# Kernel optimization log

Hardware: AMD Instinct MI355X
Metric: run time of the kernel (lower is better)

The kernel has to match this reference:

```python
import jax, jax.numpy as jnp
from jax import lax
import numpy as np

B, T, NCLS, D = 64, 2048, 20, 2048
LCS_LEN, FSD_LEN = 64, 32
LAMB1, LAMB2, LAMB3 = 1.0, 5e-5, 8e-5
LAMB_LCS, LAMB_FSD = 0.01, 0.01
FEAT_MARGIN = 50.0
THRES = 0.5
GAMMA = 0.1


def cos_sim(a, b):
    a = a / jnp.linalg.norm(a, axis=1, keepdims=True)
    b = b / jnp.linalg.norm(b, axis=1, keepdims=True)
    return a @ b.T


def dp_fsd(c0, c1):
    # soft-LCS/DTW-style recurrence with maxGamma (soft max) over 3 neighbors
    h = c0.shape[-1] // 2
    m = cos_sim(c0[:, :h], c1[:, :h])  # [L, L]
    g = cos_sim(c0[:, h:], c1[:, h:])  # [L, L]
    L = m.shape[0]

    def row_step(prev_row, mg):
        m_row, g_row = mg
        diag = prev_row[:-1]  # C[i-1, j-1]
        up = prev_row[1:]     # C[i-1, j]

        def col_step(left, xs):  # left = C[i, j-1]
            d, u, mij, gij = xs
            neigh = jnp.stack([d, gij + u, gij + left])
            val = mij + GAMMA * jax.nn.logsumexp(neigh / GAMMA)
            return val, val

        _, row_vals = lax.scan(col_step, jnp.zeros((), m.dtype), (diag, up, m_row, g_row))
        new_row = jnp.concatenate([jnp.zeros((1,), m.dtype), row_vals])
        return new_row, None

    final_row, _ = lax.scan(row_step, jnp.zeros(L + 1, m.dtype), (m, g))
    return final_row[-1]


def dp_lcs(c0, c1):
    s = cos_sim(c0, c1)  # [L, L]
    L = s.shape[0]

    def row_step(prev_row, s_row):
        diag = prev_row[:-1]
        up = prev_row[1:]

        def col_step(left, xs):
            d, u, sij = xs
            val = jnp.where(sij > THRES, d + sij, jnp.maximum(u, left))
            return val, val

        _, row_vals = lax.scan(col_step, jnp.zeros((), s.dtype), (diag, up, s_row))
        return jnp.concatenate([jnp.zeros((1,), s.dtype), row_vals]), None

    final_row, _ = lax.scan(row_step, jnp.zeros(L + 1, s.dtype), s)
    return final_row[-1]


def cls_criterion(p, lab):
    return -jnp.mean(jnp.sum(jnp.log(p + 1e-10) * lab, axis=1))


def forward_once(ai_cls, ac_cls, ab_cls, vlab, att, ai_feat, ac_feat, ab_feat, ai_cas):
    bs = ai_cls.shape[0]
    ones = jnp.ones((bs, 1), ai_cls.dtype)
    zeros = jnp.zeros((bs, 1), ai_cls.dtype)
    inst_lab = jnp.concatenate([vlab, zeros], axis=1)
    cont_lab = jnp.concatenate([vlab, ones], axis=1)
    back_lab = jnp.concatenate([jnp.zeros_like(vlab), ones], axis=1)
    inst_lab = inst_lab / jnp.sum(inst_lab, axis=1, keepdims=True)
    cont_lab = cont_lab / jnp.sum(cont_lab, axis=1, keepdims=True)
    back_lab = back_lab / jnp.sum(back_lab, axis=1, keepdims=True)

    inst_loss = cls_criterion(ai_cls, inst_lab)
    cont_loss = cls_criterion(ac_cls, cont_lab)
    back_loss = cls_criterion(ab_cls, back_lab)

    guide_loss = jnp.mean(jnp.sum(jnp.abs(1.0 - ai_cas[:, :, -1] - lax.stop_gradient(att[:, :, 0])), axis=1))

    n_inst = jnp.linalg.norm(ai_feat, axis=1)
    n_cont = jnp.linalg.norm(ac_feat, axis=1)
    n_back = jnp.linalg.norm(ab_feat, axis=1)
    f1 = jnp.maximum(FEAT_MARGIN - n_inst + n_cont, 0.0)
    f2 = jnp.maximum(FEAT_MARGIN - n_cont + n_back, 0.0)
    f3 = n_back
    feat_loss = jnp.mean((f1 + f2 + f3) ** 2)

    sparse_loss = jnp.mean(jnp.sum(att[:, :, :2], axis=1))

    cls_loss = inst_loss + cont_loss + back_loss  # THUMOS14 weights 1/1/1
    return cls_loss + LAMB1 * guide_loss + LAMB2 * feat_loss + LAMB3 * sparse_loss


def _pair_loss(vals, pair_label):
    bs = vals.shape[0]
    pos = jnp.sum(vals * pair_label)
    neg = jnp.sum(vals * (1.0 - pair_label))
    pos_num = jnp.sum(pair_label)
    neg_num = bs - pos_num
    return neg / (neg_num + 1e-10) - pos / (pos_num + 1e-10)


def ftcl_forward(act_inst_cls_0, act_cont_cls_0, act_back_cls_0, vid_label_0, temp_att_0,
                 act_inst_feat_0, act_cont_feat_0, act_back_feat_0, act_inst_cas_0,
                 lcs_candi_0, fsd_act_candi_0, fsd_bak_candi_0,
                 act_inst_cls_1, act_cont_cls_1, act_back_cls_1, vid_label_1, temp_att_1,
                 act_inst_feat_1, act_cont_feat_1, act_back_feat_1, act_inst_cas_1,
                 lcs_candi_1, fsd_act_candi_1, fsd_bak_candi_1):
    loss_0 = forward_once(act_inst_cls_0, act_cont_cls_0, act_back_cls_0, vid_label_0, temp_att_0,
                          act_inst_feat_0, act_cont_feat_0, act_back_feat_0, act_inst_cas_0)
    loss_1 = forward_once(act_inst_cls_1, act_cont_cls_1, act_back_cls_1, vid_label_1, temp_att_1,
                          act_inst_feat_1, act_cont_feat_1, act_back_feat_1, act_inst_cas_1)
    acm_loss = (loss_0 + loss_1) / 2.0

    pair_label = (jnp.sum(vid_label_0 * vid_label_1, axis=1) > 0).astype(jnp.float32)  # [B]

    lcs = jax.vmap(dp_lcs)(lcs_candi_0, lcs_candi_1)  # [B]
    lcs_loss = _pair_loss(lcs, pair_label)

    # pair==1 -> act_1, pair==0 -> bak_1 (matches the per-sample branch in torch)
    fsd_c1 = jnp.where(pair_label[:, None, None] > 0, fsd_act_candi_1, fsd_bak_candi_1)
    fsd = jax.vmap(dp_fsd)(fsd_act_candi_0, fsd_c1)  # [B]
    fsd_loss = _pair_loss(fsd, pair_label)

    return acm_loss + LAMB_LCS * lcs_loss + LAMB_FSD * fsd_loss


def setup_inputs() -> dict:
    key = jax.random.key(0)
    ks = iter(jax.random.split(key, 32))
    rand = lambda s: jax.random.uniform(next(ks), s, jnp.float32)
    randn = lambda s: jax.random.normal(next(ks), s, jnp.float32)
    inp = {}
    for sfx in ('0', '1'):
        inp[f'act_inst_cls_{sfx}'] = rand((B, NCLS + 1))
        inp[f'act_cont_cls_{sfx}'] = rand((B, NCLS + 1))
        inp[f'act_back_cls_{sfx}'] = rand((B, NCLS + 1))
        inp[f'vid_label_{sfx}'] = jnp.ones((B, NCLS), jnp.float32)
        inp[f'temp_att_{sfx}'] = rand((B, T, 3))
        inp[f'act_inst_feat_{sfx}'] = randn((B, D))
        inp[f'act_cont_feat_{sfx}'] = randn((B, D))
        inp[f'act_back_feat_{sfx}'] = randn((B, D))
        inp[f'act_inst_cas_{sfx}'] = rand((B, T, NCLS + 1))
        inp[f'lcs_candi_{sfx}'] = randn((B, LCS_LEN, D))
        inp[f'fsd_act_candi_{sfx}'] = randn((B, FSD_LEN, D))
        inp[f'fsd_bak_candi_{sfx}'] = randn((B, FSD_LEN, D))
    return inp


def reference(act_inst_cls_0, act_cont_cls_0, act_back_cls_0, vid_label_0, temp_att_0,
              act_inst_feat_0, act_cont_feat_0, act_back_feat_0, act_inst_cas_0,
              lcs_candi_0, fsd_act_candi_0, fsd_bak_candi_0,
              act_inst_cls_1, act_cont_cls_1, act_back_cls_1, vid_label_1, temp_att_1,
              act_inst_feat_1, act_cont_feat_1, act_back_feat_1, act_inst_cas_1,
              lcs_candi_1, fsd_act_candi_1, fsd_bak_candi_1):
    return ftcl_forward(act_inst_cls_0, act_cont_cls_0, act_back_cls_0, vid_label_0, temp_att_0,
                        act_inst_feat_0, act_cont_feat_0, act_back_feat_0, act_inst_cas_0,
                        lcs_candi_0, fsd_act_candi_0, fsd_bak_candi_0,
                        act_inst_cls_1, act_cont_cls_1, act_back_cls_1, vid_label_1, temp_att_1,
                        act_inst_feat_1, act_cont_feat_1, act_back_feat_1, act_inst_cas_1,
                        lcs_candi_1, fsd_act_candi_1, fsd_bak_candi_1)
```

## Files before the change

### kernel.cpp

```cpp
#include <hip/hip_runtime.h>
#include <math.h>

#define Bn 64
#define Tn 2048
#define NCLS 20
#define Dn 2048
#define LCSL 64
#define FSDL 32

typedef __bf16 bf16x4 __attribute__((ext_vector_type(4)));
typedef __bf16 bf16x8 __attribute__((ext_vector_type(8)));
typedef float f32x4 __attribute__((ext_vector_type(4)));

#define WS_LCS 0
#define WS_FSD 64
#define WS_NORM 128
#define WS_GS 512
#define WS_LSQ 1024
#define WS_FSQ 66560
#define WS_SPART 99328
#define WS_MG 2196480

__global__ __launch_bounds__(256) void mega_kernel(
    const float* __restrict__ lcs0, const float* __restrict__ lcs1,
    const float* __restrict__ fA0, const float* __restrict__ fA1,
    const float* __restrict__ fB1,
    const float* __restrict__ vid0, const float* __restrict__ vid1,
    const float* __restrict__ cas0, const float* __restrict__ att0,
    const float* __restrict__ cas1, const float* __restrict__ att1,
    const float* __restrict__ f0, const float* __restrict__ f1,
    const float* __restrict__ f2, const float* __restrict__ f3,
    const float* __restrict__ f4, const float* __restrict__ f5,
    float* __restrict__ ws) {
    __shared__ __bf16 tA[4096];
    __shared__ __bf16 tB[4096];
    const int t = threadIdx.x;
    const int bid = blockIdx.x;
    const int w = t >> 6, lane = t & 63;
    const int quad = lane >> 4, l16 = lane & 15;

    if (bid < 512) {
        const int b = bid >> 3, ks = bid & 7;
        const float* c0 = lcs0 + (size_t)b * LCSL * Dn + ks * 256;
        const float* c1 = lcs1 + (size_t)b * LCSL * Dn + ks * 256;

        f32x4 acc[4] = {};
        float sqa[4] = {0.f, 0.f, 0.f, 0.f}, sqb[4] = {0.f, 0.f, 0.f, 0.f};
        float4 pA[4], pB[4];
        #pragma unroll
        for (int l = 0; l < 4; ++l) {
            int idx4 = l * 256 + t;
            int row = idx4 >> 4, kq4 = idx4 & 15;
            pA[l] = *(const float4*)(c0 + (size_t)row * Dn + kq4 * 4);
            pB[l] = *(const float4*)(c1 + (size_t)row * Dn + kq4 * 4);
        }
        for (int kc = 0; kc < 4; ++kc) {
            __syncthreads();
            #pragma unroll
            for (int l = 0; l < 4; ++l) {
                int idx4 = l * 256 + t;
                int row = idx4 >> 4, kq4 = idx4 & 15;
                int c = kq4 >> 1, h = kq4 & 1;
                int pos = row * 64 + ((c ^ (row & 7)) << 3) + h * 4;
                float4 av = pA[l], bv = pB[l];
                bf16x4 a4 = {(__bf16)av.x, (__bf16)av.y, (__bf16)av.z, (__bf16)av.w};
                bf16x4 b4 = {(__bf16)bv.x, (__bf16)bv.y, (__bf16)bv.z, (__bf16)bv.w};
                *(bf16x4*)&tA[pos] = a4;
                *(bf16x4*)&tB[pos] = b4;
                sqa[l] += av.x * av.x + av.y * av.y + av.z * av.z + av.w * av.w;
                sqb[l] += bv.x * bv.x + bv.y * bv.y + bv.z * bv.z + bv.w * bv.w;
            }
            if (kc < 3) {
                const float* n0 = c0 + (kc + 1) * 64;
                const float* n1 = c1 + (kc + 1) * 64;
                #pragma unroll
                for (int l = 0; l < 4; ++l) {
                    int idx4 = l * 256 + t;
                    int row = idx4 >> 4, kq4 = idx4 & 15;
                    pA[l] = *(const float4*)(n0 + (size_t)row * Dn + kq4 * 4);
                    pB[l] = *(const float4*)(n1 + (size_t)row * Dn + kq4 * 4);
                }
            }
            __syncthreads();
            #pragma unroll
            for (int s = 0; s < 2; ++s) {
                int ar = w * 16 + l16;
                int ac_ = (s * 4 + quad) ^ (ar & 7);
                bf16x8 af = *(const bf16x8*)&tA[ar * 64 + (ac_ << 3)];
                #pragma unroll
                for (int tj = 0; tj < 4; ++tj) {
                    int br = tj * 16 + l16;
                    int bc = (s * 4 + quad) ^ (br & 7);
                    bf16x8 bf = *(const bf16x8*)&tB[br * 64 + (bc << 3)];
                    acc[tj] = __builtin_amdgcn_mfma_f32_16x16x32_bf16(af, bf, acc[tj], 0, 0, 0);
                }
            }
        }
        float* dst = ws + WS_SPART + (size_t)(b * 8 + ks) * 4096;
        #pragma unroll
        for (int tj = 0; tj < 4; ++tj)
            #pragma unroll
            for (int rg = 0; rg < 4; ++rg)
                dst[(w * 16 + quad * 4 + rg) * 64 + tj * 16 + l16] = acc[tj][rg];
        #pragma unroll
        for (int l = 0; l < 4; ++l) {
            float sa = sqa[l], sb = sqb[l];
            #pragma unroll
            for (int m = 1; m < 16; m <<= 1) {
                sa += __shfl_xor(sa, m);
                sb += __shfl_xor(sb, m);
            }
            if ((t & 15) == 0) {
                int r = l * 16 + (t >> 4);
                float* q = ws + WS_LSQ + (size_t)(b * 8 + ks) * 128;
                q[r] = sa;
                q[64 + r] = sb;
            }
        }
    } else if (bid < 1024) {
        const int qb = bid - 512;
        const int b = qb >> 3, half = (qb >> 2) & 1, ks = qb & 3;
        float ps = 0.f;
        for (int c = 0; c < NCLS; ++c) ps += vid0[b * NCLS + c] * vid1[b * NCLS + c];
        const float* base1 = (ps > 0.f) ? fA1 : fB1;
        const float* c0 = fA0 + (size_t)b * FSDL * Dn + half * 1024 + ks * 256;
        const float* c1 = base1 + (size_t)b * FSDL * Dn + half * 1024 + ks * 256;
        const int wi = w >> 1, wj = w & 1;

        f32x4 acc = {};
        float sqa[2] = {0.f, 0.f}, sqb[2] = {0.f, 0.f};
        float4 pA[2], pB[2];
        #pragma unroll
        for (int l = 0; l < 2; ++l) {
            int idx4 = l * 256 + t;
            int row = idx4 >> 4, kq4 = idx4 & 15;
            pA[l] = *(const float4*)(c0 + (size_t)row * Dn + kq4 * 4);
            pB[l] = *(const float4*)(c1 + (size_t)row * Dn + kq4 * 4);
        }
        for (int kc = 0; kc < 4; ++kc) {
            __syncthreads();
            #pragma unroll
            for (int l = 0; l < 2; ++l) {
                int idx4 = l * 256 + t;
                int row = idx4 >> 4, kq4 = idx4 & 15;
                int c = kq4 >> 1, h = kq4 & 1;
                int pos = row * 64 + ((c ^ (row & 7)) << 3) + h * 4;
                float4 av = pA[l], bv = pB[l];
                bf16x4 a4 = {(__bf16)av.x, (__bf16)av.y, (__bf16)av.z, (__bf16)av.w};
                bf16x4 b4 = {(__bf16)bv.x, (__bf16)bv.y, (__bf16)bv.z, (__bf16)bv.w};
                *(bf16x4*)&tA[pos] = a4;
                *(bf16x4*)&tB[pos] = b4;
                sqa[l] += av.x * av.x + av.y * av.y + av.z * av.z + av.w * av.w;
                sqb[l] += bv.x * bv.x + bv.y * bv.y + bv.z * bv.z + bv.w * bv.w;
            }
            if (kc < 3) {
                const float* n0 = c0 + (kc + 1) * 64;
                const float* n1 = c1 + (kc + 1) * 64;
                #pragma unroll
                for (int l = 0; l < 2; ++l) {
                    int idx4 = l * 256 + t;
                    int row = idx4 >> 4, kq4 = idx4 & 15;
                    pA[l] = *(const float4*)(n0 + (size_t)row * Dn + kq4 * 4);
                    pB[l] = *(const float4*)(n1 + (size_t)row * Dn + kq4 * 4);
                }
            }
            __syncthreads();
            #pragma unroll
            for (int s = 0; s < 2; ++s) {
                int ar = wi * 16 + l16;
                int ac_ = (s * 4 + quad) ^ (ar & 7);
                bf16x8 af = *(const bf16x8*)&tA[ar * 64 + (ac_ << 3)];
                int br = wj * 16 + l16;
                int bc = (s * 4 + quad) ^ (br & 7);
                bf16x8 bf = *(const bf16x8*)&tB[br * 64 + (bc << 3)];
                acc = __builtin_amdgcn_mfma_f32_16x16x32_bf16(af, bf, acc, 0, 0, 0);
            }
        }
        float* dst = ws + WS_MG + (size_t)((b * 2 + half) * 4 + ks) * 1024;
        #pragma unroll
        for (int rg = 0; rg < 4; ++rg)
            dst[(wi * 16 + quad * 4 + rg) * 32 + wj * 16 + l16] = acc[rg];
        #pragma unroll
        for (int l = 0; l < 2; ++l) {
            float sa = sqa[l], sb = sqb[l];
            #pragma unroll
            for (int m = 1; m < 16; m <<= 1) {
                sa += __shfl_xor(sa, m);
                sb += __shfl_xor(sb, m);
            }
            if ((t & 15) == 0) {
                int r = l * 16 + (t >> 4);
                float* qq = ws + WS_FSQ + (size_t)((b * 2 + half) * 4 + ks) * 64;
                qq[r] = sa;
                qq[32 + r] = sb;
            }
        }
    } else if (bid < 1152) {
        const int gb = bid - 1024;
        const int N = Bn * Tn;
        float g0 = 0.f, s0 = 0.f, g1 = 0.f, s1 = 0.f;
        for (int n = gb * 256 + t; n < 2 * N; n += 128 * 256) {
            int sfx = (n >= N);
            int m = sfx ? (n - N) : n;
            const float* cas = sfx ? cas1 : cas0;
            const float* att = sfx ? att1 : att0;
            float a0 = att[m * 3 + 0];
            float a1 = att[m * 3 + 1];
            float g = fabsf(1.0f - cas[m * (NCLS + 1) + NCLS] - a0);
            float s = a0 + a1;
            if (sfx) { g1 += g; s1 += s; } else { g0 += g; s0 += s; }
        }
        float* red = (float*)tA;
        float vals[4] = {g0, s0, g1, s1};
        #pragma unroll
        for (int v = 0; v < 4; ++v) red[v * 256 + t] = vals[v];
        __syncthreads();
        for (int o = 128; o; o >>= 1) {
            if (t < o) {
                #pragma unroll
                for (int v = 0; v < 4; ++v) red[v * 256 + t] += red[v * 256 + t + o];
            }
            __syncthreads();
        }
        if (t < 4) ws[WS_GS + gb * 4 + t] = red[t * 256];
    } else {
        int R = (bid - 1152) * 4 + w;
        const float* arr[6] = {f0, f1, f2, f3, f4, f5};
        const float* p = arr[R >> 6] + (size_t)(R & 63) * Dn;
        float s = 0.f;
        #pragma unroll
        for (int qd = 0; qd < 8; ++qd) {
            float4 v = *(const float4*)(p + qd * 256 + lane * 4);
            s += v.x * v.x + v.y * v.y + v.z * v.z + v.w * v.w;
        }
        for (int off = 32; off; off >>= 1) s += __shfl_down(s, off);
        if (lane == 0) ws[WS_NORM + R] = sqrtf(s);
    }
}

__global__ __launch_bounds__(256) void dp_kernel(float* __restrict__ ws) {
    const int t = threadIdx.x;
    if (blockIdx.x < 64) {
        const int b = blockIdx.x;
        __shared__ float S[64 * 68];
        __shared__ float inv[128];
        if (t < 128) {
            float s = 0.f;
            #pragma unroll
            for (int ks = 0; ks < 8; ++ks)
                s += ws[WS_LSQ + (size_t)(b * 8 + ks) * 128 + t];
            inv[t] = 1.0f / sqrtf(s);
        }
        __syncthreads();
        const float* sp = ws + WS_SPART + (size_t)b * 32768;
        #pragma unroll
        for (int qd = 0; qd < 4; ++qd) {
            int idx4 = qd * 256 + t;
            int i = idx4 >> 4, j = (idx4 & 15) * 4;
            float4 v = {0.f, 0.f, 0.f, 0.f};
            #pragma unroll
            for (int ks = 0; ks < 8; ++ks) {
                float4 p = *(const float4*)(sp + (size_t)ks * 4096 + idx4 * 4);
                v.x += p.x; v.y += p.y; v.z += p.z; v.w += p.w;
            }
            float ri = inv[i];
            S[i * 68 + j + 0] = v.x * ri * inv[64 + j + 0];
            S[i * 68 + j + 1] = v.y * ri * inv[64 + j + 1];
            S[i * 68 + j + 2] = v.z * ri * inv[64 + j + 2];
            S[i * 68 + j + 3] = v.w * ri * inv[64 + j + 3];
        }
        __syncthreads();
        if (t < 64) {
            float prev = 0.f, prevprev = 0.f;
            float sval_next = S[t * 68 + 0];
            for (int d = 2; d <= 128; ++d) {
                float s = sval_next;
                int jn = d - t - 1;
                if (jn >= 0 && jn < 64) sval_next = S[t * 68 + jn];
                float up = __shfl_up(prev, 1);
                float dg = __shfl_up(prevprev, 1);
                if (t == 0) { up = 0.f; dg = 0.f; }
                int j = d - t - 1;
                float left = prev;
                float val = (s > 0.5f) ? (dg + s) : fmaxf(up, left);
                float cur = (j >= 1 && j <= 64) ? val : 0.f;
                prevprev = prev;
                prev = cur;
            }
            if (t == 63) ws[WS_LCS + b] = prev;
        }
    } else {
        const int b = blockIdx.x - 64;
        __shared__ float M[32 * 36], G[32 * 36];
        __shared__ float inv[128];
        if (t < 128) {
            int half = t >> 6, sub = t & 63;
            float s = 0.f;
            #pragma unroll
            for (int ks = 0; ks < 4; ++ks)
                s += ws[WS_FSQ + (size_t)((b * 2 + half) * 4 + ks) * 64 + sub];
            inv[t] = 1.0f / sqrtf(s);
        }
        __syncthreads();
        {
            int idx4 = t;
            int i = idx4 >> 3, j = (idx4 & 7) * 4;
            float4 vM = {0.f, 0.f, 0.f, 0.f}, vG = {0.f, 0.f, 0.f, 0.f};
            #pragma unroll
            for (int ks = 0; ks < 4; ++ks) {
                float4 pM = *(const float4*)(ws + WS_MG + (size_t)((b * 2 + 0) * 4 + ks) * 1024 + idx4 * 4);
                float4 pG = *(const float4*)(ws + WS_MG + (size_t)((b * 2 + 1) * 4 + ks) * 1024 + idx4 * 4);
                vM.x += pM.x; vM.y += pM.y; vM.z += pM.z; vM.w += pM.w;
                vG.x += pG.x; vG.y += pG.y; vG.z += pG.z; vG.w += pG.w;
            }
            float riM = inv[i], riG = inv[64 + i];
            M[i * 36 + j + 0] = vM.x * riM * inv[32 + j + 0];
            M[i * 36 + j + 1] = vM.y * riM * inv[32 + j + 1];
            M[i * 36 + j + 2] = vM.z * riM * inv[32 + j + 2];
            M[i * 36 + j + 3] = vM.w * riM * inv[32 + j + 3];
            G[i * 36 + j + 0] = vG.x * riG * inv[96 + j + 0];
            G[i * 36 + j + 1] = vG.y * riG * inv[96 + j + 1];
            G[i * 36 + j + 2] = vG.z * riG * inv[96 + j + 2];
            G[i * 36 + j + 3] = vG.w * riG * inv[96 + j + 3];
        }
        __syncthreads();
        if (t < 32) {
            float prev = 0.f, prevprev = 0.f;
            float m_next = M[t * 36 + 0], g_next = G[t * 36 + 0];
            for (int d = 2; d <= 64; ++d) {
                float m = m_next, g = g_next;
                int jn = d - t - 1;
                if (jn >= 0 && jn < 32) { m_next = M[t * 36 + jn]; g_next = G[t * 36 + jn]; }
                float up = __shfl_up(prev, 1);
                float dg = __shfl_up(prevprev, 1);
                if (t == 0) { up = 0.f; dg = 0.f; }
                int j = d - t - 1;
                float left = prev;
                float x0 = dg * 10.0f;
                float x1 = (g + up) * 10.0f;
                float x2 = (g + left) * 10.0f;
                float mx = fmaxf(x0, fmaxf(x1, x2));
                float lse = mx + __logf(__expf(x0 - mx) + __expf(x1 - mx) + __expf(x2 - mx));
                float val = m + 0.1f * lse;
                float cur = (j >= 1 && j <= 32) ? val : 0.f;
                prevprev = prev;
                prev = cur;
            }
            if (t == 31) ws[WS_FSD + b] = prev;
        }
    }
}

__device__ float block_reduce(float v, float* red, int t) {
    red[t] = v;
    __syncthreads();
    for (int o = 128; o; o >>= 1) {
        if (t < o) red[t] += red[t + o];
        __syncthreads();
    }
    float r = red[0];
    __syncthreads();
    return r;
}

__global__ __launch_bounds__(256) void final_kernel(
    const float* __restrict__ ai0, const float* __restrict__ ac0,
    const float* __restrict__ ab0, const float* __restrict__ vid0,
    const float* __restrict__ ai1, const float* __restrict__ ac1,
    const float* __restrict__ ab1, const float* __restrict__ vid1,
    const float* __restrict__ ws, float* __restrict__ out) {
    __shared__ float rs0[Bn], rs1[Bn], plsh[Bn];
    __shared__ float red[256];
    int t = threadIdx.x;
    if (t < Bn) {
        float s0 = 0.f, s1 = 0.f, pp = 0.f;
        for (int c = 0; c < NCLS; ++c) {
            float a = vid0[t * NCLS + c], bl = vid1[t * NCLS + c];
            s0 += a; s1 += bl; pp += a * bl;
        }
        rs0[t] = s0;
        rs1[t] = s1;
        plsh[t] = (pp > 0.f) ? 1.f : 0.f;
    }
    __syncthreads();

    float inst0 = 0.f, cont0 = 0.f, back0 = 0.f;
    float inst1 = 0.f, cont1 = 0.f, back1 = 0.f;
    for (int idx = t; idx < Bn * (NCLS + 1); idx += 256) {
        int b = idx / (NCLS + 1), c = idx % (NCLS + 1);
        float v0 = (c < NCLS) ? vid0[b * NCLS + c] : 0.f;
        float v1 = (c < NCLS) ? vid1[b * NCLS + c] : 0.f;
        float wI0 = (c < NCLS) ? (v0 / rs0[b]) : 0.f;
        float wC0 = ((c < NCLS) ? v0 : 1.f) / (rs0[b] + 1.f);
        float wI1 = (c < NCLS) ? (v1 / rs1[b]) : 0.f;
        float wC1 = ((c < NCLS) ? v1 : 1.f) / (rs1[b] + 1.f);
        inst0 += logf(ai0[idx] + 1e-10f) * wI0;
        cont0 += logf(ac0[idx] + 1e-10f) * wC0;
        inst1 += logf(ai1[idx] + 1e-10f) * wI1;
        cont1 += logf(ac1[idx] + 1e-10f) * wC1;
        if (c == NCLS) {
            back0 += logf(ab0[idx] + 1e-10f);
            back1 += logf(ab1[idx] + 1e-10f);
        }
    }
    float sInst0 = block_reduce(inst0, red, t);
    float sCont0 = block_reduce(cont0, red, t);
    float sBack0 = block_reduce(back0, red, t);
    float sInst1 = block_reduce(inst1, red, t);
    float sCont1 = block_reduce(cont1, red, t);
    float sBack1 = block_reduce(back1, red, t);

    float g0 = 0.f, s0v = 0.f, g1 = 0.f, s1v = 0.f;
    for (int i = t; i < 128; i += 256) {
        g0  += ws[WS_GS + i * 4 + 0];
        s0v += ws[WS_GS + i * 4 + 1];
        g1  += ws[WS_GS + i * 4 + 2];
        s1v += ws[WS_GS + i * 4 + 3];
    }
    float sG0 = block_reduce(g0, red, t);
    float sS0 = block_reduce(s0v, red, t);
    float sG1 = block_reduce(g1, red, t);
    float sS1 = block_reduce(s1v, red, t);

    float fv0 = 0.f, fv1 = 0.f;
    if (t < Bn) {
        const float* nm = ws + WS_NORM;
        {
            float ni = nm[0 * Bn + t], nc = nm[1 * Bn + t], nb = nm[2 * Bn + t];
            float f1 = fmaxf(50.0f - ni + nc, 0.f);
            float f2 = fmaxf(50.0f - nc + nb, 0.f);
            float f = f1 + f2 + nb;
            fv0 = f * f;
        }
        {
            float ni = nm[3 * Bn + t], nc = nm[4 * Bn + t], nb = nm[5 * Bn + t];
            float f1 = fmaxf(50.0f - ni + nc, 0.f);
            float f2 = fmaxf(50.0f - nc + nb, 0.f);
            float f = f1 + f2 + nb;
            fv1 = f * f;
        }
    }
    float sFeat0 = block_reduce(fv0, red, t) / (float)Bn;
    float sFeat1 = block_reduce(fv1, red, t) / (float)Bn;

    float posL = 0.f, negL = 0.f, posF = 0.f, negF = 0.f, pln = 0.f;
    if (t < Bn) {
        float pl = plsh[t];
        float lv = ws[WS_LCS + t];
        float fv = ws[WS_FSD + t];
        posL = lv * pl; negL = lv * (1.f - pl);
        posF = fv * pl; negF = fv * (1.f - pl);
        pln = pl;
    }
    float sPosL = block_reduce(posL, red, t);
    float sNegL = block_reduce(negL, red, t);
    float sPosF = block_reduce(posF, red, t);
    float sNegF = block_reduce(negF, red, t);
    float sPln = block_reduce(pln, red, t);

    if (t == 0) {
        float cls0 = -(sInst0 + sCont0 + sBack0) / (float)Bn;
        float cls1 = -(sInst1 + sCont1 + sBack1) / (float)Bn;
        float guide0 = sG0 / (float)Bn;
        float sparse0 = sS0 / (float)(Bn * 2);
        float guide1 = sG1 / (float)Bn;
        float sparse1 = sS1 / (float)(Bn * 2);
        float loss0 = cls0 + 1.0f * guide0 + 5e-05f * sFeat0 + 8e-05f * sparse0;
        float loss1 = cls1 + 1.0f * guide1 + 5e-05f * sFeat1 + 8e-05f * sparse1;
        float acm = 0.5f * (loss0 + loss1);
        float posn = sPln;
        float negn = (float)Bn - posn;
        float lcs_loss = sNegL / (negn + 1e-10f) - sPosL / (posn + 1e-10f);
        float fsd_loss = sNegF / (negn + 1e-10f) - sPosF / (posn + 1e-10f);
        out[0] = acm + 0.01f * lcs_loss + 0.01f * fsd_loss;
    }
}

extern "C" void kernel_launch(void* const* d_in, const int* in_sizes, int n_in,
                              void* d_out, int out_size, void* d_ws, size_t ws_size,
                              hipStream_t stream) {
    (void)in_sizes; (void)n_in; (void)out_size; (void)ws_size;
    const float* ai0  = (const float*)d_in[0];
    const float* ac0  = (const float*)d_in[1];
    const float* ab0  = (const float*)d_in[2];
    const float* vid0 = (const float*)d_in[3];
    const float* att0 = (const float*)d_in[4];
    const float* fi0  = (const float*)d_in[5];
    const float* fc0  = (const float*)d_in[6];
    const float* fb0  = (const float*)d_in[7];
    const float* cas0 = (const float*)d_in[8];
    const float* lcs0 = (const float*)d_in[9];
    const float* fsdA0 = (const float*)d_in[10];
    const float* ai1  = (const float*)d_in[12];
    const float* ac1  = (const float*)d_in[13];
    const float* ab1  = (const float*)d_in[14];
    const float* vid1 = (const float*)d_in[15];
    const float* att1 = (const float*)d_in[16];
    const float* fi1  = (const float*)d_in[17];
    const float* fc1  = (const float*)d_in[18];
    const float* fb1  = (const float*)d_in[19];
    const float* cas1 = (const float*)d_in[20];
    const float* lcs1 = (const float*)d_in[21];
    const float* fsdA1 = (const float*)d_in[22];
    const float* fsdB1 = (const float*)d_in[23];

    float* ws = (float*)d_ws;

    mega_kernel<<<1248, 256, 0, stream>>>(lcs0, lcs1, fsdA0, fsdA1, fsdB1,
                                          vid0, vid1, cas0, att0, cas1, att1,
                                          fi0, fc0, fb0, fi1, fc1, fb1, ws);
    dp_kernel<<<128, 256, 0, stream>>>(ws);
    final_kernel<<<1, 256, 0, stream>>>(ai0, ac0, ab0, vid0, ai1, ac1, ab1, vid1, ws,
                                        (float*)d_out);
}
```

Measured before the change: 239.5 us.

## Double-buffer LDS tiles, templatize K-split count, and batch final reductions

The GEMM-like similarity stages now use double-buffered shared-memory tiles, so the next chunk is written while the current one feeds MFMA, and one barrier per iteration is removed. The K-split count becomes a template parameter, and NS=16 is chosen when the workspace is large enough. That doubles the number of blocks for the LCS and FSD partial products, at the cost of more partial-sum traffic into the dp_kernel reduction. The final kernel merges its scalar block reductions into float4 reductions to cut the number of barrier-heavy reduction passes.

```diff
diff --git a/kernel.cpp b/kernel.cpp
--- a/kernel.cpp
+++ b/kernel.cpp
@@ -16,11 +16,16 @@
 #define WS_FSD 64
 #define WS_NORM 128
 #define WS_GS 512
-#define WS_LSQ 1024
-#define WS_FSQ 66560
-#define WS_SPART 99328
-#define WS_MG 2196480
-
+template <int NS>
+struct WsOff {
+    static constexpr size_t LSQ = 1024;
+    static constexpr size_t FSQ = LSQ + (size_t)64 * NS * 128;
+    static constexpr size_t SPART = FSQ + (size_t)64 * NS * 64;
+    static constexpr size_t MG = SPART + (size_t)64 * NS * 4096;
+    static constexpr size_t END = MG + (size_t)64 * NS * 1024;
+};
+
+template <int NS>
 __global__ __launch_bounds__(256) void mega_kernel(
     const float* __restrict__ lcs0, const float* __restrict__ lcs1,
     const float* __restrict__ fA0, const float* __restrict__ fA1,
@@ -32,30 +37,35 @@
     const float* __restrict__ f2, const float* __restrict__ f3,
     const float* __restrict__ f4, const float* __restrict__ f5,
     float* __restrict__ ws) {
-    __shared__ __bf16 tA[4096];
-    __shared__ __bf16 tB[4096];
+    constexpr int L = (NS == 16) ? 4 : 3;
+    constexpr int KC = 2048 / NS / 64;
+    using O = WsOff<NS>;
+    __shared__ __align__(16) __bf16 tA[2][4096];
+    __shared__ __align__(16) __bf16 tB[2][4096];
     const int t = threadIdx.x;
     const int bid = blockIdx.x;
     const int w = t >> 6, lane = t & 63;
     const int quad = lane >> 4, l16 = lane & 15;
 
-    if (bid < 512) {
-        const int b = bid >> 3, ks = bid & 7;
-        const float* c0 = lcs0 + (size_t)b * LCSL * Dn + ks * 256;
-        const float* c1 = lcs1 + (size_t)b * LCSL * Dn + ks * 256;
+    if (bid < 64 * NS) {
+        const int b = bid >> L, ks = bid & (NS - 1);
+        const float* c0 = lcs0 + (size_t)b * LCSL * Dn + ks * (2048 / NS);
+        const float* c1 = lcs1 + (size_t)b * LCSL * Dn + ks * (2048 / NS);
 
         f32x4 acc[4] = {};
         float sqa[4] = {0.f, 0.f, 0.f, 0.f}, sqb[4] = {0.f, 0.f, 0.f, 0.f};
         float4 pA[4], pB[4];
-        #pragma unroll
-        for (int l = 0; l < 4; ++l) {
-            int idx4 = l * 256 + t;
-            int row = idx4 >> 4, kq4 = idx4 & 15;
-            pA[l] = *(const float4*)(c0 + (size_t)row * Dn + kq4 * 4);
-            pB[l] = *(const float4*)(c1 + (size_t)row * Dn + kq4 * 4);
-        }
-        for (int kc = 0; kc < 4; ++kc) {
-            __syncthreads();
+
+        auto LOADL = [&](int st) {
+            #pragma unroll
+            for (int l = 0; l < 4; ++l) {
+                int idx4 = l * 256 + t;
+                int row = idx4 >> 4, kq4 = idx4 & 15;
+                pA[l] = *(const float4*)(c0 + (size_t)row * Dn + st * 64 + kq4 * 4);
+                pB[l] = *(const float4*)(c1 + (size_t)row * Dn + st * 64 + kq4 * 4);
+            }
+        };
+        auto WRITEL = [&](int buf) {
             #pragma unroll
             for (int l = 0; l < 4; ++l) {
                 int idx4 = l * 256 + t;
@@ -65,38 +75,39 @@
                 float4 av = pA[l], bv = pB[l];
                 bf16x4 a4 = {(__bf16)av.x, (__bf16)av.y, (__bf16)av.z, (__bf16)av.w};
                 bf16x4 b4 = {(__bf16)bv.x, (__bf16)bv.y, (__bf16)bv.z, (__bf16)bv.w};
-                *(bf16x4*)&tA[pos] = a4;
-                *(bf16x4*)&tB[pos] = b4;
+                *(bf16x4*)&tA[buf][pos] = a4;
+                *(bf16x4*)&tB[buf][pos] = b4;
                 sqa[l] += av.x * av.x + av.y * av.y + av.z * av.z + av.w * av.w;
                 sqb[l] += bv.x * bv.x + bv.y * bv.y + bv.z * bv.z + bv.w * bv.w;
             }
-            if (kc < 3) {
-                const float* n0 = c0 + (kc + 1) * 64;
-                const float* n1 = c1 + (kc + 1) * 64;
-                #pragma unroll
-                for (int l = 0; l < 4; ++l) {
-                    int idx4 = l * 256 + t;
-                    int row = idx4 >> 4, kq4 = idx4 & 15;
-                    pA[l] = *(const float4*)(n0 + (size_t)row * Dn + kq4 * 4);
-                    pB[l] = *(const float4*)(n1 + (size_t)row * Dn + kq4 * 4);
-                }
-            }
-            __syncthreads();
+        };
+
+        LOADL(0);
+        WRITEL(0);
+        if (KC > 1) LOADL(1);
+        __syncthreads();
+        for (int kc = 0; kc < KC; ++kc) {
+            const int cur = kc & 1;
             #pragma unroll
             for (int s = 0; s < 2; ++s) {
                 int ar = w * 16 + l16;
                 int ac_ = (s * 4 + quad) ^ (ar & 7);
-                bf16x8 af = *(const bf16x8*)&tA[ar * 64 + (ac_ << 3)];
+                bf16x8 af = *(const bf16x8*)&tA[cur][ar * 64 + (ac_ << 3)];
                 #pragma unroll
                 for (int tj = 0; tj < 4; ++tj) {
                     int br = tj * 16 + l16;
                     int bc = (s * 4 + quad) ^ (br & 7);
-                    bf16x8 bf = *(const bf16x8*)&tB[br * 64 + (bc << 3)];
+                    bf16x8 bf = *(const bf16x8*)&tB[cur][br * 64 + (bc << 3)];
                     acc[tj] = __builtin_amdgcn_mfma_f32_16x16x32_bf16(af, bf, acc[tj], 0, 0, 0);
                 }
             }
-        }
-        float* dst = ws + WS_SPART + (size_t)(b * 8 + ks) * 4096;
+            if (kc + 1 < KC) {
+                WRITEL(cur ^ 1);
+                if (kc + 2 < KC) LOADL(kc + 2);
+                __syncthreads();
+            }
+        }
+        float* dst = ws + O::SPART + (size_t)(b * NS + ks) * 4096;
         #pragma unroll
         for (int tj = 0; tj < 4; ++tj)
             #pragma unroll
@@ -112,33 +123,38 @@
             }
             if ((t & 15) == 0) {
                 int r = l * 16 + (t >> 4);
-                float* q = ws + WS_LSQ + (size_t)(b * 8 + ks) * 128;
+                float* q = ws + O::LSQ + (size_t)(b * NS + ks) * 128;
                 q[r] = sa;
                 q[64 + r] = sb;
             }
         }
-    } else if (bid < 1024) {
-        const int qb = bid - 512;
-        const int b = qb >> 3, half = (qb >> 2) & 1, ks = qb & 3;
+    } else if (bid < 128 * NS) {
+        const int qb = bid - 64 * NS;
+        const int b = qb >> L;
+        const int idx = qb & (NS - 1);
+        const int half = idx >> (L - 1);
+        const int ks = idx & (NS / 2 - 1);
         float ps = 0.f;
         for (int c = 0; c < NCLS; ++c) ps += vid0[b * NCLS + c] * vid1[b * NCLS + c];
         const float* base1 = (ps > 0.f) ? fA1 : fB1;
-        const float* c0 = fA0 + (size_t)b * FSDL * Dn + half * 1024 + ks * 256;
-        const float* c1 = base1 + (size_t)b * FSDL * Dn + half * 1024 + ks * 256;
+        const float* c0 = fA0 + (size_t)b * FSDL * Dn + half * 1024 + ks * (2048 / NS);
+        const float* c1 = base1 + (size_t)b * FSDL * Dn + half * 1024 + ks * (2048 / NS);
         const int wi = w >> 1, wj = w & 1;
 
         f32x4 acc = {};
         float sqa[2] = {0.f, 0.f}, sqb[2] = {0.f, 0.f};
         float4 pA[2], pB[2];
-        #pragma unroll
-        for (int l = 0; l < 2; ++l) {
-            int idx4 = l * 256 + t;
-            int row = idx4 >> 4, kq4 = idx4 & 15;
-            pA[l] = *(const float4*)(c0 + (size_t)row * Dn + kq4 * 4);
-            pB[l] = *(const float4*)(c1 + (size_t)row * Dn + kq4 * 4);
-        }
-        for (int kc = 0; kc < 4; ++kc) {
-            __syncthreads();
+
+        auto LOADF = [&](int st) {
+            #pragma unroll
+            for (int l = 0; l < 2; ++l) {
+                int idx4 = l * 256 + t;
+                int row = idx4 >> 4, kq4 = idx4 & 15;
+                pA[l] = *(const float4*)(c0 + (size_t)row * Dn + st * 64 + kq4 * 4);
+                pB[l] = *(const float4*)(c1 + (size_t)row * Dn + st * 64 + kq4 * 4);
+            }
+        };
+        auto WRITEF = [&](int buf) {
             #pragma unroll
             for (int l = 0; l < 2; ++l) {
                 int idx4 = l * 256 + t;
@@ -148,35 +164,36 @@
                 float4 av = pA[l], bv = pB[l];
                 bf16x4 a4 = {(__bf16)av.x, (__bf16)av.y, (__bf16)av.z, (__bf16)av.w};
                 bf16x4 b4 = {(__bf16)bv.x, (__bf16)bv.y, (__bf16)bv.z, (__bf16)bv.w};
-                *(bf16x4*)&tA[pos] = a4;
-                *(bf16x4*)&tB[pos] = b4;
+                *(bf16x4*)&tA[buf][pos] = a4;
+                *(bf16x4*)&tB[buf][pos] = b4;
                 sqa[l] += av.x * av.x + av.y * av.y + av.z * av.z + av.w * av.w;
                 sqb[l] += bv.x * bv.x + bv.y * bv.y + bv.z * bv.z + bv.w * bv.w;
             }
-            if (kc < 3) {
-                const float* n0 = c0 + (kc + 1) * 64;
-                const float* n1 = c1 + (kc + 1) * 64;
-                #pragma unroll
-                for (int l = 0; l < 2; ++l) {
-                    int idx4 = l * 256 + t;
-                    int row = idx4 >> 4, kq4 = idx4 & 15;
-                    pA[l] = *(const float4*)(n0 + (size_t)row * Dn + kq4 * 4);
-                    pB[l] = *(const float4*)(n1 + (size_t)row * Dn + kq4 * 4);
-                }
-            }
-            __syncthreads();
+        };
+
+        LOADF(0);
+        WRITEF(0);
+        if (KC > 1) LOADF(1);
+        __syncthreads();
+        for (int kc = 0; kc < KC; ++kc) {
+            const int cur = kc & 1;
             #pragma unroll
             for (int s = 0; s < 2; ++s) {
                 int ar = wi * 16 + l16;
                 int ac_ = (s * 4 + quad) ^ (ar & 7);
-                bf16x8 af = *(const bf16x8*)&tA[ar * 64 + (ac_ << 3)];
+                bf16x8 af = *(const bf16x8*)&tA[cur][ar * 64 + (ac_ << 3)];
                 int br = wj * 16 + l16;
                 int bc = (s * 4 + quad) ^ (br & 7);
-                bf16x8 bf = *(const bf16x8*)&tB[br * 64 + (bc << 3)];
+                bf16x8 bf = *(const bf16x8*)&tB[cur][br * 64 + (bc << 3)];
                 acc = __builtin_amdgcn_mfma_f32_16x16x32_bf16(af, bf, acc, 0, 0, 0);
             }
-        }
-        float* dst = ws + WS_MG + (size_t)((b * 2 + half) * 4 + ks) * 1024;
+            if (kc + 1 < KC) {
+                WRITEF(cur ^ 1);
+                if (kc + 2 < KC) LOADF(kc + 2);
+                __syncthreads();
+            }
+        }
+        float* dst = ws + O::MG + (size_t)((b * 2 + half) * (NS / 2) + ks) * 1024;
         #pragma unroll
         for (int rg = 0; rg < 4; ++rg)
             dst[(wi * 16 + quad * 4 + rg) * 32 + wj * 16 + l16] = acc[rg];
@@ -190,13 +207,13 @@
             }
             if ((t & 15) == 0) {
                 int r = l * 16 + (t >> 4);
-                float* qq = ws + WS_FSQ + (size_t)((b * 2 + half) * 4 + ks) * 64;
+                float* qq = ws + O::FSQ + (size_t)((b * 2 + half) * (NS / 2) + ks) * 64;
                 qq[r] = sa;
                 qq[32 + r] = sb;
             }
         }
-    } else if (bid < 1152) {
-        const int gb = bid - 1024;
+    } else if (bid < 128 * NS + 128) {
+        const int gb = bid - 128 * NS;
         const int N = Bn * Tn;
         float g0 = 0.f, s0 = 0.f, g1 = 0.f, s1 = 0.f;
         for (int n = gb * 256 + t; n < 2 * N; n += 128 * 256) {
@@ -224,7 +241,7 @@
         }
         if (t < 4) ws[WS_GS + gb * 4 + t] = red[t * 256];
     } else {
-        int R = (bid - 1152) * 4 + w;
+        int R = (bid - (128 * NS + 128)) * 4 + w;
         const float* arr[6] = {f0, f1, f2, f3, f4, f5};
         const float* p = arr[R >> 6] + (size_t)(R & 63) * Dn;
         float s = 0.f;
@@ -238,7 +255,9 @@
     }
 }
 
+template <int NS>
 __global__ __launch_bounds__(256) void dp_kernel(float* __restrict__ ws) {
+    using O = WsOff<NS>;
     const int t = threadIdx.x;
     if (blockIdx.x < 64) {
         const int b = blockIdx.x;
@@ -247,19 +266,19 @@
         if (t < 128) {
             float s = 0.f;
             #pragma unroll
-            for (int ks = 0; ks < 8; ++ks)
-                s += ws[WS_LSQ + (size_t)(b * 8 + ks) * 128 + t];
+            for (int ks = 0; ks < NS; ++ks)
+                s += ws[O::LSQ + (size_t)(b * NS + ks) * 128 + t];
             inv[t] = 1.0f / sqrtf(s);
         }
         __syncthreads();
-        const float* sp = ws + WS_SPART + (size_t)b * 32768;
+        const float* sp = ws + O::SPART + (size_t)b * NS * 4096;
         #pragma unroll
         for (int qd = 0; qd < 4; ++qd) {
             int idx4 = qd * 256 + t;
             int i = idx4 >> 4, j = (idx4 & 15) * 4;
             float4 v = {0.f, 0.f, 0.f, 0.f};
             #pragma unroll
-            for (int ks = 0; ks < 8; ++ks) {
+            for (int ks = 0; ks < NS; ++ks) {
                 float4 p = *(const float4*)(sp + (size_t)ks * 4096 + idx4 * 4);
                 v.x += p.x; v.y += p.y; v.z += p.z; v.w += p.w;
             }
@@ -297,8 +316,8 @@
             int half = t >> 6, sub = t & 63;
             float s = 0.f;
             #pragma unroll
-            for (int ks = 0; ks < 4; ++ks)
-                s += ws[WS_FSQ + (size_t)((b * 2 + half) * 4 + ks) * 64 + sub];
+            for (int ks = 0; ks < NS / 2; ++ks)
+                s += ws[O::FSQ + (size_t)((b * 2 + half) * (NS / 2) + ks) * 64 + sub];
             inv[t] = 1.0f / sqrtf(s);
         }
         __syncthreads();
@@ -307,9 +326,9 @@
             int i = idx4 >> 3, j = (idx4 & 7) * 4;
             float4 vM = {0.f, 0.f, 0.f, 0.f}, vG = {0.f, 0.f, 0.f, 0.f};
             #pragma unroll
-            for (int ks = 0; ks < 4; ++ks) {
-                float4 pM = *(const float4*)(ws + WS_MG + (size_t)((b * 2 + 0) * 4 + ks) * 1024 + idx4 * 4);
-                float4 pG = *(const float4*)(ws + WS_MG + (size_t)((b * 2 + 1) * 4 + ks) * 1024 + idx4 * 4);
+            for (int ks = 0; ks < NS / 2; ++ks) {
+                float4 pM = *(const float4*)(ws + O::MG + (size_t)((b * 2 + 0) * (NS / 2) + ks) * 1024 + idx4 * 4);
+                float4 pG = *(const float4*)(ws + O::MG + (size_t)((b * 2 + 1) * (NS / 2) + ks) * 1024 + idx4 * 4);
                 vM.x += pM.x; vM.y += pM.y; vM.z += pM.z; vM.w += pM.w;
                 vG.x += pG.x; vG.y += pG.y; vG.z += pG.z; vG.w += pG.w;
             }
@@ -351,14 +370,19 @@
     }
 }
 
-__device__ float block_reduce(float v, float* red, int t) {
+__device__ __forceinline__ float4 block_reduce4(float4 v, float4* red, int t) {
     red[t] = v;
     __syncthreads();
     for (int o = 128; o; o >>= 1) {
-        if (t < o) red[t] += red[t + o];
-        __syncthreads();
-    }
-    float r = red[0];
+        if (t < o) {
+            red[t].x += red[t + o].x;
+            red[t].y += red[t + o].y;
+            red[t].z += red[t + o].z;
+            red[t].w += red[t + o].w;
+        }
+        __syncthreads();
+    }
+    float4 r = red[0];
     __syncthreads();
     return r;
 }
@@ -370,7 +394,7 @@
     const float* __restrict__ ab1, const float* __restrict__ vid1,
     const float* __restrict__ ws, float* __restrict__ out) {
     __shared__ float rs0[Bn], rs1[Bn], plsh[Bn];
-    __shared__ float red[256];
+    __shared__ __align__(16) float4 red[256];
     int t = threadIdx.x;
     if (t < Bn) {
         float s0 = 0.f, s1 = 0.f, pp = 0.f;
@@ -403,12 +427,6 @@
             back1 += logf(ab1[idx] + 1e-10f);
         }
     }
-    float sInst0 = block_reduce(inst0, red, t);
-    float sCont0 = block_reduce(cont0, red, t);
-    float sBack0 = block_reduce(back0, red, t);
-    float sInst1 = block_reduce(inst1, red, t);
-    float sCont1 = block_reduce(cont1, red, t);
-    float sBack1 = block_reduce(back1, red, t);
 
     float g0 = 0.f, s0v = 0.f, g1 = 0.f, s1v = 0.f;
     for (int i = t; i < 128; i += 256) {
@@ -417,10 +435,6 @@
         g1  += ws[WS_GS + i * 4 + 2];
         s1v += ws[WS_GS + i * 4 + 3];
     }
-    float sG0 = block_reduce(g0, red, t);
-    float sS0 = block_reduce(s0v, red, t);
-    float sG1 = block_reduce(g1, red, t);
-    float sS1 = block_reduce(s1v, red, t);
 
     float fv0 = 0.f, fv1 = 0.f;
     if (t < Bn) {
@@ -440,8 +454,6 @@
             fv1 = f * f;
         }
     }
-    float sFeat0 = block_reduce(fv0, red, t) / (float)Bn;
-    float sFeat1 = block_reduce(fv1, red, t) / (float)Bn;
 
     float posL = 0.f, negL = 0.f, posF = 0.f, negF = 0.f, pln = 0.f;
     if (t < Bn) {
@@ -452,26 +464,29 @@
         posF = fv * pl; negF = fv * (1.f - pl);
         pln = pl;
     }
-    float sPosL = block_reduce(posL, red, t);
-    float sNegL = block_reduce(negL, red, t);
-    float sPosF = block_reduce(posF, red, t);
-    float sNegF = block_reduce(negF, red, t);
-    float sPln = block_reduce(pln, red, t);
+
+    float4 r1 = block_reduce4({inst0, cont0, back0, inst1}, red, t);
+    float4 r2 = block_reduce4({cont1, back1, g0, s0v}, red, t);
+    float4 r3 = block_reduce4({g1, s1v, fv0, fv1}, red, t);
+    float4 r4 = block_reduce4({posL, negL, posF, negF}, red, t);
+    float4 r5 = block_reduce4({pln, 0.f, 0.f, 0.f}, red, t);
 
     if (t == 0) {
-        float cls0 = -(sInst0 + sCont0 + sBack0) / (float)Bn;
-        float cls1 = -(sInst1 + sCont1 + sBack1) / (float)Bn;
-        float guide0 = sG0 / (float)Bn;
-        float sparse0 = sS0 / (float)(Bn * 2);
-        float guide1 = sG1 / (float)Bn;
-        float sparse1 = sS1 / (float)(Bn * 2);
+        float cls0 = -(r1.x + r1.y + r1.z) / (float)Bn;
+        float cls1 = -(r1.w + r2.x + r2.y) / (float)Bn;
+        float guide0 = r2.z / (float)Bn;
+        float sparse0 = r2.w / (float)(Bn * 2);
+        float guide1 = r3.x / (float)Bn;
+        float sparse1 = r3.y / (float)(Bn * 2);
+        float sFeat0 = r3.z / (float)Bn;
+        float sFeat1 = r3.w / (float)Bn;
         float loss0 = cls0 + 1.0f * guide0 + 5e-05f * sFeat0 + 8e-05f * sparse0;
         float loss1 = cls1 + 1.0f * guide1 + 5e-05f * sFeat1 + 8e-05f * sparse1;
         float acm = 0.5f * (loss0 + loss1);
-        float posn = sPln;
+        float posn = r5.x;
         float negn = (float)Bn - posn;
-        float lcs_loss = sNegL / (negn + 1e-10f) - sPosL / (posn + 1e-10f);
-        float fsd_loss = sNegF / (negn + 1e-10f) - sPosF / (posn + 1e-10f);
+        float lcs_loss = r4.y / (negn + 1e-10f) - r4.x / (posn + 1e-10f);
+        float fsd_loss = r4.w / (negn + 1e-10f) - r4.z / (posn + 1e-10f);
         out[0] = acm + 0.01f * lcs_loss + 0.01f * fsd_loss;
     }
 }
@@ -479,7 +494,7 @@
 extern "C" void kernel_launch(void* const* d_in, const int* in_sizes, int n_in,
                               void* d_out, int out_size, void* d_ws, size_t ws_size,
                               hipStream_t stream) {
-    (void)in_sizes; (void)n_in; (void)out_size; (void)ws_size;
+    (void)in_sizes; (void)n_in; (void)out_size;
     const float* ai0  = (const float*)d_in[0];
     const float* ac0  = (const float*)d_in[1];
     const float* ab0  = (const float*)d_in[2];
@@ -506,10 +521,17 @@
 
     float* ws = (float*)d_ws;
 
-    mega_kernel<<<1248, 256, 0, stream>>>(lcs0, lcs1, fsdA0, fsdA1, fsdB1,
-                                          vid0, vid1, cas0, att0, cas1, att1,
-                                          fi0, fc0, fb0, fi1, fc1, fb1, ws);
-    dp_kernel<<<128, 256, 0, stream>>>(ws);
+    if (ws_size >= WsOff<16>::END * sizeof(float)) {
+        mega_kernel<16><<<128 * 16 + 224, 256, 0, stream>>>(
+            lcs0, lcs1, fsdA0, fsdA1, fsdB1, vid0, vid1, cas0, att0, cas1, att1,
+            fi0, fc0, fb0, fi1, fc1, fb1, ws);
+        dp_kernel<16><<<128, 256, 0, stream>>>(ws);
+    } else {
+        mega_kernel<8><<<128 * 8 + 224, 256, 0, stream>>>(
+            lcs0, lcs1, fsdA0, fsdA1, fsdB1, vid0, vid1, cas0, att0, cas1, att1,
+            fi0, fc0, fb0, fi1, fc1, fb1, ws);
+        dp_kernel<8><<<128, 256, 0, stream>>>(ws);
+    }
     final_kernel<<<1, 256, 0, stream>>>(ai0, ac0, ab0, vid0, ai1, ac1, ab1, vid1, ws,
                                         (float*)d_out);
 }
```

After: 236.0 us. About the same (-1.5%).
